# Performance work log

Hardware: AMD Instinct MI355X
Metric: run time of the kernel (lower is better)

The kernel has to match this reference:

```python
import jax, jax.numpy as jnp
import numpy as np

D = 1024
H = 16
HD = D // H
EPS = 1e-5
NEG = -1e20


def _layernorm(x, w, b):
    m = jnp.mean(x, axis=-1, keepdims=True)
    v = jnp.mean((x - m) ** 2, axis=-1, keepdims=True)
    return (x - m) * jax.lax.rsqrt(v + EPS) * w + b


def setup_inputs() -> dict:
    key = jax.random.key(0)
    ks = jax.random.split(key, 16)
    s = 0.02
    inp = {
        "X": jax.random.normal(ks[0], (2, 2048, D), jnp.float32),
        "Wq": jax.random.normal(ks[1], (D, D), jnp.float32) * s,
        "bq": jnp.zeros((D,), jnp.float32),
        "Wk": jax.random.normal(ks[2], (D, D), jnp.float32) * s,
        "bk": jnp.zeros((D,), jnp.float32),
        "Wv": jax.random.normal(ks[3], (D, D), jnp.float32) * s,
        "bv": jnp.zeros((D,), jnp.float32),
        "Wo": jax.random.normal(ks[4], (D, D), jnp.float32) * s,
        "bo": jnp.zeros((D,), jnp.float32),
        "ln1_w": jnp.ones((D,), jnp.float32),
        "ln1_b": jnp.zeros((D,), jnp.float32),
        "Wup": jax.random.normal(ks[5], (4 * D, D), jnp.float32) * s,
        "bup": jnp.zeros((4 * D,), jnp.float32),
        "Wdown": jax.random.normal(ks[6], (D, 4 * D), jnp.float32) * s,
        "bdown": jnp.zeros((D,), jnp.float32),
        "ln2_w": jnp.ones((D,), jnp.float32),
        "ln2_b": jnp.zeros((D,), jnp.float32),
    }
    return inp


def reference(X, Wq, bq, Wk, bk, Wv, bv, Wo, bo, ln1_w, ln1_b,
              Wup, bup, Wdown, bdown, ln2_w, ln2_b):
    B, S, _ = X.shape
    # QKV projections -> [B, H, S, HD]
    q = (X @ Wq.T + bq).reshape(B, S, H, HD).transpose(0, 2, 1, 3)
    k = (X @ Wk.T + bk).reshape(B, S, H, HD).transpose(0, 2, 1, 3)
    v = (X @ Wv.T + bv).reshape(B, S, H, HD).transpose(0, 2, 1, 3)
    scores = jnp.einsum("bhqd,bhkd->bhqk", q, k) / jnp.sqrt(jnp.float32(HD))
    causal = jnp.tril(jnp.ones((S, S), dtype=bool))  # mask==0 -> -1e20
    scores = jnp.where(causal, scores, jnp.float32(NEG))
    attn = jax.nn.softmax(scores, axis=-1)  # dropout is identity in eval
    out = jnp.einsum("bhqk,bhkd->bhqd", attn, v)
    out = out.transpose(0, 2, 1, 3).reshape(B, S, D)
    out = out @ Wo.T + bo
    x = _layernorm(X + out, ln1_w, ln1_b)  # post-LN attention block
    up = jax.nn.relu(x @ Wup.T + bup)
    down = up @ Wdown.T + bdown
    return _layernorm(x + down, ln2_w, ln2_b)
```

## Files before the change

### kernel.cpp

```cpp
#include <hip/hip_runtime.h>
#include <stdint.h>

#define DMODEL 1024
#define NHEAD 16
#define HDIM 64
#define SEQ 2048
#define NBATCH 2
#define MTOK 4096

typedef float f32x4 __attribute__((ext_vector_type(4)));
typedef short s16x8 __attribute__((ext_vector_type(8)));
typedef unsigned short u16;
typedef u16 u16x4 __attribute__((ext_vector_type(4)));

typedef __attribute__((address_space(1))) const void* as1_cvp;
typedef __attribute__((address_space(3))) void* as3_vp;

__device__ inline u16 f2bf(float f) {
  uint32_t u = __float_as_uint(f);
  u = u + 0x7FFFu + ((u >> 16) & 1u);
  return (u16)(u >> 16);
}

__device__ inline void gload_lds16(const void* g, void* l) {
  __builtin_amdgcn_global_load_lds((as1_cvp)g, (as3_vp)l, 16, 0, 0);
}

__global__ __launch_bounds__(256) void k_f2bf(const float* __restrict__ src,
                                              u16* __restrict__ dst, int n4) {
  int i = blockIdx.x * 256 + threadIdx.x;
  int stride = gridDim.x * 256;
  for (; i < n4; i += stride) {
    f32x4 v = ((const f32x4*)src)[i];
    u16x4 o;
    o[0] = f2bf(v[0]); o[1] = f2bf(v[1]); o[2] = f2bf(v[2]); o[3] = f2bf(v[3]);
    ((u16x4*)dst)[i] = o;
  }
}

__global__ __launch_bounds__(256) void k_f2bf_w4(
    const float* __restrict__ s0, const float* __restrict__ s1,
    const float* __restrict__ s2, const float* __restrict__ s3,
    u16* __restrict__ d0, u16* __restrict__ d1, u16* __restrict__ d2,
    u16* __restrict__ d3, int n4) {
  const float* src = blockIdx.y == 0 ? s0 : blockIdx.y == 1 ? s1
                     : blockIdx.y == 2 ? s2 : s3;
  u16* dst = blockIdx.y == 0 ? d0 : blockIdx.y == 1 ? d1
             : blockIdx.y == 2 ? d2 : d3;
  int i = blockIdx.x * 256 + threadIdx.x;
  int stride = gridDim.x * 256;
  for (; i < n4; i += stride) {
    f32x4 v = ((const f32x4*)src)[i];
    u16x4 o;
    o[0] = f2bf(v[0]); o[1] = f2bf(v[1]); o[2] = f2bf(v[2]); o[3] = f2bf(v[3]);
    ((u16x4*)dst)[i] = o;
  }
}

template <int MODE, int KSPL, int MH>
__global__ __launch_bounds__(512, 2) void k_gemm256(
    const u16* __restrict__ A, const u16* __restrict__ B,
    const float* __restrict__ bias, void* __restrict__ Cv,
    void* __restrict__ Cv1, int M, int N, int K) {
  constexpr int HALVES = MH + 2;
  __shared__ alignas(16) u16 lds[2 * HALVES * 8192];
  const int t = threadIdx.x;
  const int w = t >> 6;
  const int l = t & 63;
  const int wr = w >> 2;
  const int wc = w & 3;
  const int lr = l & 15, lg = l >> 4;
  const int r7 = lr & 7;
  const int lrow8 = l >> 3;

  const int gx = gridDim.x;
  int lin = blockIdx.y * gx + blockIdx.x;
  const int nwg = gx * gridDim.y;
  lin = (lin & 7) * (nwg >> 3) + (lin >> 3);
  const int bx = lin % gx, by = lin / gx;
  const int kz = KSPL > 1 ? blockIdx.z : 0;
  const int Kc = K / KSPL, kbeg = kz * Kc;
  const int brow = by * (MH * 128), bcol = bx * 256;

  constexpr int MF = MH * 4;
  const f32x4 Z4 = {0.f, 0.f, 0.f, 0.f};
  f32x4 acc[MF][4];
#pragma unroll
  for (int m = 0; m < MF; m++)
#pragma unroll
    for (int n = 0; n < 4; n++) acc[m][n] = Z4;

  const u16* Ag = A + (size_t)brow * K + kbeg;
  const u16* Bg = B + (size_t)bcol * K + kbeg;
  const int swz_src = ((l & 7) ^ ((l >> 3) & 7)) << 3;

  auto ldsH = [&](int buf, int half) { return lds + (buf * HALVES + half) * 8192; };
  auto stageA = [&](int kt, int buf) {
#pragma unroll
    for (int h = 0; h < MH; h++) {
      u16* lb = ldsH(buf, h);
      const int rb = h * 128;
      gload_lds16(Ag + (size_t)(rb + w * 8 + lrow8) * K + kt * 64 + swz_src,
                  lb + w * 512);
      gload_lds16(Ag + (size_t)(rb + 64 + w * 8 + lrow8) * K + kt * 64 + swz_src,
                  lb + (8 + w) * 512);
    }
  };
  auto stageB = [&](int kt, int buf) {
#pragma unroll
    for (int h = 0; h < 2; h++) {
      u16* lb = ldsH(buf, MH + h);
      const int rb = h * 128;
      gload_lds16(Bg + (size_t)(rb + w * 8 + lrow8) * K + kt * 64 + swz_src,
                  lb + w * 512);
      gload_lds16(Bg + (size_t)(rb + 64 + w * 8 + lrow8) * K + kt * 64 + swz_src,
                  lb + (8 + w) * 512);
    }
  };

  stageA(0, 0);
  stageB(0, 0);

  const int nkt = Kc >> 6;
  const int arb = (MH == 2) ? 0 : wr * 64;
  const int brb = (wc & 1) * 64;
  for (int kt = 0; kt < nkt; ++kt) {
    const int cur = kt & 1, nx = cur ^ 1;
    if (kt + 1 < nkt) {
      stageA(kt + 1, nx);
      if (MH == 2)
        asm volatile("s_waitcnt vmcnt(4)" ::: "memory");
      else
        asm volatile("s_waitcnt vmcnt(2)" ::: "memory");
    } else {
      asm volatile("s_waitcnt vmcnt(0)" ::: "memory");
    }
    __builtin_amdgcn_s_barrier();
    __builtin_amdgcn_sched_barrier(0);
    const u16* Ah = ldsH(cur, (MH == 2) ? wr : 0);
    const u16* Bh = ldsH(cur, MH + (wc >> 1));
#pragma unroll
    for (int kk = 0; kk < 2; kk++) {
      s16x8 bfr[4];
#pragma unroll
      for (int nf = 0; nf < 4; nf++)
        bfr[nf] = *(const s16x8*)(Bh + (brb + nf * 16 + lr) * 64 +
                                  (((kk * 4 + lg) ^ r7) << 3));
#pragma unroll
      for (int mh = 0; mh < MH; mh++) {
        s16x8 afr[4];
#pragma unroll
        for (int i = 0; i < 4; i++)
          afr[i] = *(const s16x8*)(Ah + (arb + (mh * 4 + i) * 16 + lr) * 64 +
                                   (((kk * 4 + lg) ^ r7) << 3));
        __builtin_amdgcn_s_setprio(1);
#pragma unroll
        for (int i = 0; i < 4; i++)
#pragma unroll
          for (int nf = 0; nf < 4; nf++)
            acc[mh * 4 + i][nf] = __builtin_amdgcn_mfma_f32_16x16x32_bf16(
                afr[i], bfr[nf], acc[mh * 4 + i][nf], 0, 0, 0);
        __builtin_amdgcn_s_setprio(0);
      }
      if (kk == 0 && kt + 1 < nkt) stageB(kt + 1, nx);
    }
    __builtin_amdgcn_sched_barrier(0);
    __builtin_amdgcn_s_barrier();
  }

  const int lg4 = lg * 4;
  const int wrb = wr * (MH == 2 ? 128 : 64);
  if (MODE == 0) {
    float* Co = (kz == 0) ? (float*)Cv : (float*)Cv1;
#pragma unroll
    for (int nf = 0; nf < 4; nf++) {
      const int col = bcol + wc * 64 + nf * 16 + lr;
      const float bvv = (kz == 0) ? bias[col] : 0.0f;
#pragma unroll
      for (int mf = 0; mf < MF; mf++) {
        const int row0 = brow + wrb + mf * 16 + lg4;
#pragma unroll
        for (int r = 0; r < 4; r++)
          Co[(size_t)(row0 + r) * N + col] = acc[mf][nf][r] + bvv;
      }
    }
  } else {
    u16* Sgw = lds + w * 2176;
    float bn[4];
#pragma unroll
    for (int nf = 0; nf < 4; nf++) bn[nf] = bias[bcol + wc * 64 + nf * 16 + lr];
    const int ch = l & 7;
#pragma unroll
    for (int hh = 0; hh < MH * 2; hh++) {
#pragma unroll
      for (int mm = 0; mm < 2; mm++) {
        const int mf = hh * 2 + mm;
#pragma unroll
        for (int nf = 0; nf < 4; nf++)
#pragma unroll
          for (int r = 0; r < 4; r++) {
            float vv = acc[mf][nf][r] + bn[nf];
            if (MODE == 2) vv = vv > 0.f ? vv : 0.f;
            Sgw[(mm * 16 + lg4 + r) * 68 + nf * 16 + lr] = f2bf(vv);
          }
      }
#pragma unroll
      for (int i = 0; i < 4; i++) {
        const int rr = i * 8 + (l >> 3);
        u16x4 a0 = *(const u16x4*)(Sgw + rr * 68 + ch * 8);
        u16x4 a1 = *(const u16x4*)(Sgw + rr * 68 + ch * 8 + 4);
        s16x8 v8;
#pragma unroll
        for (int j = 0; j < 4; j++) { v8[j] = (short)a0[j]; v8[4 + j] = (short)a1[j]; }
        *(s16x8*)((u16*)Cv + (size_t)(brow + wrb + hh * 32 + rr) * N +
                  (bcol + wc * 64 + ch * 8)) = v8;
      }
    }
  }
}

__global__ __launch_bounds__(256, 3) void k_gemm_qkv(
    const u16* __restrict__ A, const u16* __restrict__ B,
    const float* __restrict__ bq, const float* __restrict__ bk,
    const float* __restrict__ bv, u16* __restrict__ qbf, u16* __restrict__ kbf,
    u16* __restrict__ vtbf, int M, int N, int K) {
  __shared__ alignas(16) u16 As[2][128 * 32];
  __shared__ alignas(16) u16 Bs[2][128 * 32];
  __shared__ alignas(16) u16 Sg[4][32][68];
  const int t = threadIdx.x;
  const int w = t >> 6;
  const int l = t & 63;
  const int brow = blockIdx.y * 128;
  const int bcol = blockIdx.x * 128;
  const int wr = (w >> 1) * 64;
  const int wc = (w & 1) * 64;

  const f32x4 Z4 = {0.f, 0.f, 0.f, 0.f};
  f32x4 acc[4][4];
  for (int m = 0; m < 4; m++)
    for (int n = 0; n < 4; n++) acc[m][n] = Z4;

  const int sr = t >> 2;
  const int sc = (t & 3) * 8;
  const u16* Ab = A + (size_t)(brow + sr) * K + sc;
  const u16* Bb = B + (size_t)(bcol + sr) * K + sc;

  const int lr = l & 15;
  const int lk = (l >> 4) * 8;

  gload_lds16(Ab, &As[0][0] + w * 512);
  gload_lds16(Ab + (size_t)64 * K, &As[0][0] + 2048 + w * 512);
  gload_lds16(Bb, &Bs[0][0] + w * 512);
  gload_lds16(Bb + (size_t)64 * K, &Bs[0][0] + 2048 + w * 512);

  const int nk = K / 32;
  int cur = 0;
  for (int kt = 0; kt < nk; ++kt) {
    if (kt + 1 < nk) {
      const int k0 = (kt + 1) * 32;
      const int nx = cur ^ 1;
      gload_lds16(Ab + k0, &As[nx][0] + w * 512);
      gload_lds16(Ab + k0 + (size_t)64 * K, &As[nx][0] + 2048 + w * 512);
      gload_lds16(Bb + k0, &Bs[nx][0] + w * 512);
      gload_lds16(Bb + k0 + (size_t)64 * K, &Bs[nx][0] + 2048 + w * 512);
      asm volatile("s_waitcnt vmcnt(4)" ::: "memory");
    } else {
      asm volatile("s_waitcnt vmcnt(0)" ::: "memory");
    }
    __builtin_amdgcn_s_barrier();
    __builtin_amdgcn_sched_barrier(0);
    s16x8 af[4], bf[4];
    for (int m = 0; m < 4; m++)
      af[m] = *(const s16x8*)(&As[cur][0] + (wr + m * 16 + lr) * 32 + lk);
    for (int n = 0; n < 4; n++)
      bf[n] = *(const s16x8*)(&Bs[cur][0] + (wc + n * 16 + lr) * 32 + lk);
    for (int m = 0; m < 4; m++)
      for (int n = 0; n < 4; n++)
        acc[m][n] = __builtin_amdgcn_mfma_f32_16x16x32_bf16(af[m], bf[n],
                                                            acc[m][n], 0, 0, 0);
    __builtin_amdgcn_sched_barrier(0);
    __builtin_amdgcn_s_barrier();
    cur ^= 1;
  }

  const int lg = (l >> 4) * 4;
  const int region = bcol >> 10;
  float bn[4];
  {
    const float* bb = region == 0 ? bq : region == 1 ? bk : bv;
    for (int n = 0; n < 4; n++) bn[n] = bb[(bcol + wc + n * 16 + lr) & 1023];
  }
  if (region <= 1) {
    for (int hh = 0; hh < 2; hh++) {
      for (int mm = 0; mm < 2; mm++) {
        const int m = 2 * hh + mm;
        for (int n = 0; n < 4; n++)
          for (int r = 0; r < 4; r++) {
            float vv = acc[m][n][r] + bn[n];
            if (region == 0) vv *= 0.125f;
            Sg[w][mm * 16 + lg + r][n * 16 + lr] = f2bf(vv);
          }
      }
      const int ch = l & 7;
      for (int i = 0; i < 4; i++) {
        const int rr = i * 8 + (l >> 3);
        u16x4 a0 = *(const u16x4*)&Sg[w][rr][ch * 8];
        u16x4 a1 = *(const u16x4*)&Sg[w][rr][ch * 8 + 4];
        s16x8 v8;
        for (int j = 0; j < 4; j++) { v8[j] = (short)a0[j]; v8[4 + j] = (short)a1[j]; }
        const int tok = brow + wr + hh * 32 + rr;
        if (region == 0) {
          *(s16x8*)(qbf + (size_t)tok * 1024 + bcol + wc + ch * 8) = v8;
        } else {
          const int colb = bcol - 1024 + wc;
          *(s16x8*)(kbf + (size_t)tok * 1024 + colb + (((ch ^ tok) & 7) << 3)) =
              v8;
        }
      }
    }
  } else {
    for (int hh = 0; hh < 2; hh++) {
      for (int nn = 0; nn < 2; nn++) {
        const int n = 2 * hh + nn;
        for (int m = 0; m < 4; m++)
          for (int r = 0; r < 4; r++)
            Sg[w][nn * 16 + lr][m * 16 + lg + r] = f2bf(acc[m][n][r] + bn[n]);
      }
      const int ch = l & 7;
      const int hcol = (bcol - 2048 + wc) >> 6;
      for (int i = 0; i < 4; i++) {
        const int rr = i * 8 + (l >> 3);
        u16x4 a0 = *(const u16x4*)&Sg[w][rr][ch * 8];
        u16x4 a1 = *(const u16x4*)&Sg[w][rr][ch * 8 + 4];
        s16x8 v8;
        for (int j = 0; j < 4; j++) { v8[j] = (short)a0[j]; v8[4 + j] = (short)a1[j]; }
        const int d = hh * 32 + rr;
        const int tokb = brow + wr + ch * 8;
        const int b = tokb >> 11, s64b = tokb & 2047;
        const int ssb = (s64b & ~63) + ((((s64b >> 3) ^ d) & 7) << 3);
        *(s16x8*)(vtbf + ((size_t)((b << 4) + hcol) * 64 + d) * 2048 + ssb) = v8;
      }
    }
  }
}

__global__ __launch_bounds__(256, 2) void k_attn(const u16* __restrict__ q,
                                                 const u16* __restrict__ kk,
                                                 const u16* __restrict__ vt,
                                                 u16* __restrict__ o) {
  __shared__ alignas(16) u16 Ks[2][64 * 64];
  __shared__ alignas(16) u16 Vs[2][64 * 64];
  __shared__ alignas(16) u16 Ps[4 * 16 * 64];
  const int t = threadIdx.x;
  const int w = t >> 6;
  const int l = t & 63;
  const int idx = blockIdx.x;
  const int bh = idx & 31;
  const int p = idx >> 5;
  const int pm = p >> 3, pj = p & 7;
  const int qt = pm * 8 + ((pm & 1) ? (7 - pj) : pj);
  const int b = bh >> 4, h = bh & 15;
  const u16* qb = q + (size_t)b * SEQ * DMODEL + h * HDIM;
  const u16* kb = kk + (size_t)b * SEQ * DMODEL + h * HDIM;
  const u16* vb = vt + (size_t)((b * 16 + h) * 64) * SEQ;

  const int sr = t >> 3;
  const int sc = (t & 7) * 8;
  gload_lds16(qb + (size_t)(qt * 64 + sr) * DMODEL + sc, Ps + w * 512);
  gload_lds16(qb + (size_t)(qt * 64 + sr + 32) * DMODEL + sc,
              Ps + 2048 + w * 512);
  gload_lds16(kb + (size_t)sr * DMODEL + sc, &Ks[0][0] + w * 512);
  gload_lds16(kb + (size_t)(sr + 32) * DMODEL + sc, &Ks[0][0] + 2048 + w * 512);
  gload_lds16(vb + (size_t)sr * SEQ + sc, &Vs[0][0] + w * 512);
  gload_lds16(vb + (size_t)(sr + 32) * SEQ + sc, &Vs[0][0] + 2048 + w * 512);

  const int lr = l & 15, lg = l >> 4;
  const int key = lr & 7;
  const f32x4 Z4 = {0.f, 0.f, 0.f, 0.f};
  float m_l = -3.0e38f, l_l = 0.f;
  f32x4 oacc[4];
  for (int m = 0; m < 4; m++) oacc[m] = Z4;
  s16x8 bq0, bq1;
  u16* PsW = Ps + w * 1024;

  for (int jt = 0; jt <= qt; jt++) {
    const int cur = jt & 1;
    if (jt < qt) {
      const int nx = cur ^ 1;
      gload_lds16(kb + (size_t)((jt + 1) * 64 + sr) * DMODEL + sc,
                  &Ks[nx][0] + w * 512);
      gload_lds16(kb + (size_t)((jt + 1) * 64 + sr + 32) * DMODEL + sc,
                  &Ks[nx][0] + 2048 + w * 512);
      gload_lds16(vb + (size_t)sr * SEQ + (jt + 1) * 64 + sc,
                  &Vs[nx][0] + w * 512);
      gload_lds16(vb + (size_t)(sr + 32) * SEQ + (jt + 1) * 64 + sc,
                  &Vs[nx][0] + 2048 + w * 512);
      asm volatile("s_waitcnt vmcnt(4)" ::: "memory");
    } else {
      asm volatile("s_waitcnt vmcnt(0)" ::: "memory");
    }
    __builtin_amdgcn_s_barrier();
    __builtin_amdgcn_sched_barrier(0);
    const u16* Kc = &Ks[cur][0];
    const u16* Vc = &Vs[cur][0];
    if (jt == 0) {
      bq0 = *(const s16x8*)(Ps + (w * 16 + lr) * 64 + lg * 8);
      bq1 = *(const s16x8*)(Ps + (w * 16 + lr) * 64 + 32 + lg * 8);
    }
    f32x4 sacc[4];
    for (int m = 0; m < 4; m++) sacc[m] = Z4;
    for (int m = 0; m < 4; m++) {
      s16x8 ak0 = *(const s16x8*)(Kc + (m * 16 + lr) * 64 + ((lg ^ key) << 3));
      s16x8 ak1 =
          *(const s16x8*)(Kc + (m * 16 + lr) * 64 + (((4 | lg) ^ key) << 3));
      sacc[m] = __builtin_amdgcn_mfma_f32_16x16x32_bf16(ak0, bq0, sacc[m], 0, 0, 0);
      sacc[m] = __builtin_amdgcn_mfma_f32_16x16x32_bf16(ak1, bq1, sacc[m], 0, 0, 0);
    }
    if (jt == qt) {
      const int q_rel = w * 16 + lr;
      for (int m = 0; m < 4; m++)
        for (int r = 0; r < 4; r++)
          if (m * 16 + lg * 4 + r > q_rel) sacc[m][r] = -3.0e38f;
    }
    float tmax = -3.0e38f;
    for (int m = 0; m < 4; m++)
      for (int r = 0; r < 4; r++) tmax = fmaxf(tmax, sacc[m][r]);
    tmax = fmaxf(tmax, __shfl_xor(tmax, 16, 64));
    tmax = fmaxf(tmax, __shfl_xor(tmax, 32, 64));
    const float m_new = fmaxf(m_l, tmax);
    const float alpha = __expf(m_l - m_new);
    m_l = m_new;
    float p_[4][4];
    float rs = 0.f;
    for (int m = 0; m < 4; m++)
      for (int r = 0; r < 4; r++) {
        const float e = __expf(sacc[m][r] - m_new);
        p_[m][r] = e;
        rs += e;
      }
    rs += __shfl_xor(rs, 16, 64);
    rs += __shfl_xor(rs, 32, 64);
    l_l = l_l * alpha + rs;
    for (int m = 0; m < 4; m++)
      for (int r = 0; r < 4; r++) oacc[m][r] *= alpha;
    for (int m = 0; m < 4; m++)
      for (int pr = 0; pr < 2; pr++) {
        const uint32_t pk = (uint32_t)f2bf(p_[m][2 * pr]) |
                            ((uint32_t)f2bf(p_[m][2 * pr + 1]) << 16);
        const int kv0 = m * 16 + lg * 4 + 2 * pr;
        ((uint32_t*)PsW)[lr * 32 + (((kv0 >> 3) ^ key) << 2) +
                         ((kv0 >> 1) & 3)] = pk;
      }
    __builtin_amdgcn_sched_barrier(0);
    s16x8 bp0 = *(const s16x8*)(PsW + lr * 64 + ((lg ^ key) << 3));
    s16x8 bp1 = *(const s16x8*)(PsW + lr * 64 + (((4 | lg) ^ key) << 3));
    for (int m = 0; m < 4; m++) {
      s16x8 av0 = *(const s16x8*)(Vc + (m * 16 + lr) * 64 + ((lg ^ key) << 3));
      s16x8 av1 =
          *(const s16x8*)(Vc + (m * 16 + lr) * 64 + (((4 | lg) ^ key) << 3));
      oacc[m] = __builtin_amdgcn_mfma_f32_16x16x32_bf16(av0, bp0, oacc[m], 0, 0, 0);
      oacc[m] = __builtin_amdgcn_mfma_f32_16x16x32_bf16(av1, bp1, oacc[m], 0, 0, 0);
    }
    __builtin_amdgcn_sched_barrier(0);
    __builtin_amdgcn_s_barrier();
  }
  const float rl = 1.0f / l_l;
  const int tok = qt * 64 + w * 16 + lr;
  u16* orow = o + (size_t)(b * SEQ + tok) * DMODEL + h * HDIM;
  for (int m = 0; m < 4; m++)
    for (int pr = 0; pr < 2; pr++) {
      const uint32_t pk = (uint32_t)f2bf(oacc[m][2 * pr] * rl) |
                          ((uint32_t)f2bf(oacc[m][2 * pr + 1] * rl) << 16);
      *(uint32_t*)(orow + m * 16 + lg * 4 + 2 * pr) = pk;
    }
}

__global__ __launch_bounds__(256) void k_add_ln(const float* __restrict__ X,
                                                const float* __restrict__ Y,
                                                const float* __restrict__ Y1,
                                                const float* __restrict__ w,
                                                const float* __restrict__ bias,
                                                float* __restrict__ of32,
                                                u16* __restrict__ obf) {
  __shared__ float sred[4];
  const int t = threadIdx.x;
  const size_t row = blockIdx.x;
  f32x4 xv = ((const f32x4*)(X + row * DMODEL))[t];
  f32x4 yv = ((const f32x4*)(Y + row * DMODEL))[t];
  f32x4 vv;
  for (int i = 0; i < 4; i++) vv[i] = xv[i] + yv[i];
  if (Y1) {
    f32x4 y1 = ((const f32x4*)(Y1 + row * DMODEL))[t];
    for (int i = 0; i < 4; i++) vv[i] += y1[i];
  }
  float s = vv[0] + vv[1] + vv[2] + vv[3];
  for (int off = 32; off >= 1; off >>= 1) s += __shfl_xor(s, off, 64);
  if ((t & 63) == 0) sred[t >> 6] = s;
  __syncthreads();
  s = sred[0] + sred[1] + sred[2] + sred[3];
  const float mean = s * (1.0f / DMODEL);
  f32x4 dv;
  for (int i = 0; i < 4; i++) dv[i] = vv[i] - mean;
  float ss = dv[0] * dv[0] + dv[1] * dv[1] + dv[2] * dv[2] + dv[3] * dv[3];
  __syncthreads();
  for (int off = 32; off >= 1; off >>= 1) ss += __shfl_xor(ss, off, 64);
  if ((t & 63) == 0) sred[t >> 6] = ss;
  __syncthreads();
  ss = sred[0] + sred[1] + sred[2] + sred[3];
  const float rs = rsqrtf(ss * (1.0f / DMODEL) + 1e-5f);
  f32x4 wv = ((const f32x4*)w)[t];
  f32x4 bv = ((const f32x4*)bias)[t];
  f32x4 ov;
  for (int i = 0; i < 4; i++) ov[i] = dv[i] * rs * wv[i] + bv[i];
  if (of32) ((f32x4*)(of32 + row * DMODEL))[t] = ov;
  if (obf) {
    u16x4 ob;
    for (int i = 0; i < 4; i++) ob[i] = f2bf(ov[i]);
    ((u16x4*)(obf + row * DMODEL))[t] = ob;
  }
}

extern "C" void kernel_launch(void* const* d_in, const int* in_sizes, int n_in,
                              void* d_out, int out_size, void* d_ws,
                              size_t ws_size, hipStream_t stream) {
  const float* X = (const float*)d_in[0];
  const float* Wq = (const float*)d_in[1];
  const float* bq = (const float*)d_in[2];
  const float* Wk = (const float*)d_in[3];
  const float* bk = (const float*)d_in[4];
  const float* Wv = (const float*)d_in[5];
  const float* bvp = (const float*)d_in[6];
  const float* Wo = (const float*)d_in[7];
  const float* bo = (const float*)d_in[8];
  const float* ln1w = (const float*)d_in[9];
  const float* ln1b = (const float*)d_in[10];
  const float* Wup = (const float*)d_in[11];
  const float* bup = (const float*)d_in[12];
  const float* Wdown = (const float*)d_in[13];
  const float* bdown = (const float*)d_in[14];
  const float* ln2w = (const float*)d_in[15];
  const float* ln2b = (const float*)d_in[16];

  char* ws = (char*)d_ws;
  const size_t MB = 1024 * 1024;
  u16* Xbf = (u16*)(ws + 0);
  u16* qbf = (u16*)(ws + 8 * MB);
  u16* kbf = (u16*)(ws + 16 * MB);
  u16* vtbf = (u16*)(ws + 24 * MB);
  u16* wqkv = (u16*)(ws + 32 * MB);
  u16* wo = (u16*)(ws + 38 * MB);
  u16* attnb = (u16*)(ws + 40 * MB);
  float* Ybuf = (float*)(ws + 48 * MB);
  float* xres = (float*)(ws + 64 * MB);
  u16* xbf = (u16*)(ws + 80 * MB);
  u16* upbf = (u16*)(ws + 0);
  u16* wbig = (u16*)(ws + 32 * MB);
  float* Ypart = (float*)d_out;

  const dim3 blk(256);
  k_f2bf<<<2048, blk, 0, stream>>>(X, Xbf, (MTOK * DMODEL) / 4);
  k_f2bf_w4<<<dim3(512, 4), blk, 0, stream>>>(
      Wq, Wk, Wv, Wo, wqkv + 0 * 1024 * 1024, wqkv + 1 * 1024 * 1024,
      wqkv + 2 * 1024 * 1024, wo, (DMODEL * DMODEL) / 4);

  const dim3 gqkv(3 * DMODEL / 128, MTOK / 128);
  k_gemm_qkv<<<gqkv, blk, 0, stream>>>(Xbf, wqkv, bq, bk, bvp, qbf, kbf, vtbf,
                                       MTOK, 3 * DMODEL, DMODEL);
  k_attn<<<NBATCH * NHEAD * (SEQ / 64), blk, 0, stream>>>(qbf, kbf, vtbf, attnb);
  k_gemm256<0, 2, 1><<<dim3(4, 32, 2), dim3(512), 0, stream>>>(
      attnb, wo, bo, Ybuf, Ypart, MTOK, DMODEL, DMODEL);
  k_add_ln<<<MTOK, blk, 0, stream>>>(X, Ybuf, Ypart, ln1w, ln1b, xres, xbf);

  k_f2bf<<<2048, blk, 0, stream>>>(Wup, wbig, (4 * DMODEL * DMODEL) / 4);
  k_gemm256<2, 1, 2><<<dim3(16, 16), dim3(512), 0, stream>>>(
      xbf, wbig, bup, upbf, nullptr, MTOK, 4 * DMODEL, DMODEL);
  k_f2bf<<<2048, blk, 0, stream>>>(Wdown, wbig, (4 * DMODEL * DMODEL) / 4);
  k_gemm256<0, 2, 1><<<dim3(4, 32, 2), dim3(512), 0, stream>>>(
      upbf, wbig, bdown, Ybuf, Ypart, MTOK, DMODEL, 4 * DMODEL);
  k_add_ln<<<MTOK, blk, 0, stream>>>(xres, Ybuf, Ypart, ln2w, ln2b,
                                     (float*)d_out, (u16*)nullptr);
}
```

Baseline: 216.8 us.

## Retile QKV GEMM to 128x256 swizzled tiles and add lazy softmax rescale

Replaces the 128x128, 256-thread QKV projection GEMM with a 512-thread 128x256 tile kernel. It uses K=64 stages, XOR-swizzled LDS, split A/B prefetch interleaved with the MFMA work, s_setprio around the MFMAs, and a grouped block-index remap for L2 locality. The attention kernel's online softmax now rescales the running max and accumulators only when some lane's new max exceeds the old one by more than 8. This skips the exp and multiplies on most tiles, at the risk of larger intermediate exponentials (bounded by e^8) in bf16/fp32.

```diff
diff --git a/kernel.cpp b/kernel.cpp
--- a/kernel.cpp
+++ b/kernel.cpp
@@ -219,123 +219,169 @@
   }
 }
 
-__global__ __launch_bounds__(256, 3) void k_gemm_qkv(
+__global__ __launch_bounds__(512, 2) void k_gemm256_qkv(
     const u16* __restrict__ A, const u16* __restrict__ B,
     const float* __restrict__ bq, const float* __restrict__ bk,
     const float* __restrict__ bv, u16* __restrict__ qbf, u16* __restrict__ kbf,
     u16* __restrict__ vtbf, int M, int N, int K) {
-  __shared__ alignas(16) u16 As[2][128 * 32];
-  __shared__ alignas(16) u16 Bs[2][128 * 32];
-  __shared__ alignas(16) u16 Sg[4][32][68];
+  __shared__ alignas(16) u16 lds[2 * 3 * 8192];
   const int t = threadIdx.x;
-  const int w = t >> 6;
-  const int l = t & 63;
-  const int brow = blockIdx.y * 128;
-  const int bcol = blockIdx.x * 128;
-  const int wr = (w >> 1) * 64;
-  const int wc = (w & 1) * 64;
+  const int w = t >> 6, l = t & 63;
+  const int wr = w >> 2, wc = w & 3;
+  const int lr = l & 15, lg = l >> 4;
+  const int r7 = lr & 7;
+  const int lrow8 = l >> 3;
+
+  const int gx = gridDim.x;
+  int lin = blockIdx.y * gx + blockIdx.x;
+  const int nwg = gx * gridDim.y;
+  lin = (lin & 7) * (nwg >> 3) + (lin >> 3);
+  const int bx = lin % gx, by = lin / gx;
+  const int brow = by * 128, bcol = bx * 256;
 
   const f32x4 Z4 = {0.f, 0.f, 0.f, 0.f};
   f32x4 acc[4][4];
+#pragma unroll
   for (int m = 0; m < 4; m++)
+#pragma unroll
     for (int n = 0; n < 4; n++) acc[m][n] = Z4;
 
-  const int sr = t >> 2;
-  const int sc = (t & 3) * 8;
-  const u16* Ab = A + (size_t)(brow + sr) * K + sc;
-  const u16* Bb = B + (size_t)(bcol + sr) * K + sc;
-
-  const int lr = l & 15;
-  const int lk = (l >> 4) * 8;
-
-  gload_lds16(Ab, &As[0][0] + w * 512);
-  gload_lds16(Ab + (size_t)64 * K, &As[0][0] + 2048 + w * 512);
-  gload_lds16(Bb, &Bs[0][0] + w * 512);
-  gload_lds16(Bb + (size_t)64 * K, &Bs[0][0] + 2048 + w * 512);
-
-  const int nk = K / 32;
-  int cur = 0;
-  for (int kt = 0; kt < nk; ++kt) {
-    if (kt + 1 < nk) {
-      const int k0 = (kt + 1) * 32;
-      const int nx = cur ^ 1;
-      gload_lds16(Ab + k0, &As[nx][0] + w * 512);
-      gload_lds16(Ab + k0 + (size_t)64 * K, &As[nx][0] + 2048 + w * 512);
-      gload_lds16(Bb + k0, &Bs[nx][0] + w * 512);
-      gload_lds16(Bb + k0 + (size_t)64 * K, &Bs[nx][0] + 2048 + w * 512);
-      asm volatile("s_waitcnt vmcnt(4)" ::: "memory");
+  const u16* Ag = A + (size_t)brow * K;
+  const u16* Bg = B + (size_t)bcol * K;
+  const int swz_src = ((l & 7) ^ ((l >> 3) & 7)) << 3;
+
+  auto ldsH = [&](int buf, int half) { return lds + (buf * 3 + half) * 8192; };
+  auto stageA = [&](int kt, int buf) {
+    u16* lb = ldsH(buf, 0);
+    gload_lds16(Ag + (size_t)(w * 8 + lrow8) * K + kt * 64 + swz_src,
+                lb + w * 512);
+    gload_lds16(Ag + (size_t)(64 + w * 8 + lrow8) * K + kt * 64 + swz_src,
+                lb + (8 + w) * 512);
+  };
+  auto stageB = [&](int kt, int buf) {
+#pragma unroll
+    for (int h = 0; h < 2; h++) {
+      u16* lb = ldsH(buf, 1 + h);
+      const int rb = h * 128;
+      gload_lds16(Bg + (size_t)(rb + w * 8 + lrow8) * K + kt * 64 + swz_src,
+                  lb + w * 512);
+      gload_lds16(Bg + (size_t)(rb + 64 + w * 8 + lrow8) * K + kt * 64 + swz_src,
+                  lb + (8 + w) * 512);
+    }
+  };
+
+  stageA(0, 0);
+  stageB(0, 0);
+
+  const int nkt = K >> 6;
+  const int arb = wr * 64;
+  const int brb = (wc & 1) * 64;
+  for (int kt = 0; kt < nkt; ++kt) {
+    const int cur = kt & 1, nx = cur ^ 1;
+    if (kt + 1 < nkt) {
+      stageA(kt + 1, nx);
+      asm volatile("s_waitcnt vmcnt(2)" ::: "memory");
     } else {
       asm volatile("s_waitcnt vmcnt(0)" ::: "memory");
     }
     __builtin_amdgcn_s_barrier();
     __builtin_amdgcn_sched_barrier(0);
-    s16x8 af[4], bf[4];
-    for (int m = 0; m < 4; m++)
-      af[m] = *(const s16x8*)(&As[cur][0] + (wr + m * 16 + lr) * 32 + lk);
-    for (int n = 0; n < 4; n++)
-      bf[n] = *(const s16x8*)(&Bs[cur][0] + (wc + n * 16 + lr) * 32 + lk);
-    for (int m = 0; m < 4; m++)
-      for (int n = 0; n < 4; n++)
-        acc[m][n] = __builtin_amdgcn_mfma_f32_16x16x32_bf16(af[m], bf[n],
-                                                            acc[m][n], 0, 0, 0);
+    const u16* Ah = ldsH(cur, 0);
+    const u16* Bh = ldsH(cur, 1 + (wc >> 1));
+#pragma unroll
+    for (int kk = 0; kk < 2; kk++) {
+      s16x8 bfr[4];
+#pragma unroll
+      for (int nf = 0; nf < 4; nf++)
+        bfr[nf] = *(const s16x8*)(Bh + (brb + nf * 16 + lr) * 64 +
+                                  (((kk * 4 + lg) ^ r7) << 3));
+      s16x8 afr[4];
+#pragma unroll
+      for (int i = 0; i < 4; i++)
+        afr[i] = *(const s16x8*)(Ah + (arb + i * 16 + lr) * 64 +
+                                 (((kk * 4 + lg) ^ r7) << 3));
+      __builtin_amdgcn_s_setprio(1);
+#pragma unroll
+      for (int i = 0; i < 4; i++)
+#pragma unroll
+        for (int nf = 0; nf < 4; nf++)
+          acc[i][nf] = __builtin_amdgcn_mfma_f32_16x16x32_bf16(
+              afr[i], bfr[nf], acc[i][nf], 0, 0, 0);
+      __builtin_amdgcn_s_setprio(0);
+      if (kk == 0 && kt + 1 < nkt) stageB(kt + 1, nx);
+    }
     __builtin_amdgcn_sched_barrier(0);
     __builtin_amdgcn_s_barrier();
-    cur ^= 1;
-  }
-
-  const int lg = (l >> 4) * 4;
-  const int region = bcol >> 10;
+  }
+
+  const int lg4 = lg * 4;
+  const int wrb = wr * 64;
+  u16* Sgw = lds + w * 2176;
+  const int colw = bcol + wc * 64;
+  const int region = colw >> 10;
+  const int ck0 = colw & 1023;
   float bn[4];
   {
     const float* bb = region == 0 ? bq : region == 1 ? bk : bv;
-    for (int n = 0; n < 4; n++) bn[n] = bb[(bcol + wc + n * 16 + lr) & 1023];
-  }
+#pragma unroll
+    for (int nf = 0; nf < 4; nf++) bn[nf] = bb[ck0 + nf * 16 + lr];
+  }
+  const int ch = l & 7;
   if (region <= 1) {
+#pragma unroll
     for (int hh = 0; hh < 2; hh++) {
+#pragma unroll
       for (int mm = 0; mm < 2; mm++) {
-        const int m = 2 * hh + mm;
-        for (int n = 0; n < 4; n++)
+        const int mf = hh * 2 + mm;
+#pragma unroll
+        for (int nf = 0; nf < 4; nf++)
+#pragma unroll
           for (int r = 0; r < 4; r++) {
-            float vv = acc[m][n][r] + bn[n];
+            float vv = acc[mf][nf][r] + bn[nf];
             if (region == 0) vv *= 0.125f;
-            Sg[w][mm * 16 + lg + r][n * 16 + lr] = f2bf(vv);
+            Sgw[(mm * 16 + lg4 + r) * 68 + nf * 16 + lr] = f2bf(vv);
           }
       }
-      const int ch = l & 7;
+#pragma unroll
       for (int i = 0; i < 4; i++) {
         const int rr = i * 8 + (l >> 3);
-        u16x4 a0 = *(const u16x4*)&Sg[w][rr][ch * 8];
-        u16x4 a1 = *(const u16x4*)&Sg[w][rr][ch * 8 + 4];
+        u16x4 a0 = *(const u16x4*)(Sgw + rr * 68 + ch * 8);
+        u16x4 a1 = *(const u16x4*)(Sgw + rr * 68 + ch * 8 + 4);
         s16x8 v8;
+#pragma unroll
         for (int j = 0; j < 4; j++) { v8[j] = (short)a0[j]; v8[4 + j] = (short)a1[j]; }
-        const int tok = brow + wr + hh * 32 + rr;
-        if (region == 0) {
-          *(s16x8*)(qbf + (size_t)tok * 1024 + bcol + wc + ch * 8) = v8;
-        } else {
-          const int colb = bcol - 1024 + wc;
-          *(s16x8*)(kbf + (size_t)tok * 1024 + colb + (((ch ^ tok) & 7) << 3)) =
+        const int tok = brow + wrb + hh * 32 + rr;
+        if (region == 0)
+          *(s16x8*)(qbf + (size_t)tok * 1024 + ck0 + ch * 8) = v8;
+        else
+          *(s16x8*)(kbf + (size_t)tok * 1024 + ck0 + (((ch ^ tok) & 7) << 3)) =
               v8;
-        }
       }
     }
   } else {
+    const int hcol = ck0 >> 6;
+#pragma unroll
     for (int hh = 0; hh < 2; hh++) {
+#pragma unroll
       for (int nn = 0; nn < 2; nn++) {
-        const int n = 2 * hh + nn;
-        for (int m = 0; m < 4; m++)
+        const int nf = 2 * hh + nn;
+#pragma unroll
+        for (int mf = 0; mf < 4; mf++)
+#pragma unroll
           for (int r = 0; r < 4; r++)
-            Sg[w][nn * 16 + lr][m * 16 + lg + r] = f2bf(acc[m][n][r] + bn[n]);
-      }
-      const int ch = l & 7;
-      const int hcol = (bcol - 2048 + wc) >> 6;
+            Sgw[(nn * 16 + lr) * 68 + mf * 16 + lg4 + r] =
+                f2bf(acc[mf][nf][r] + bn[nf]);
+      }
+#pragma unroll
       for (int i = 0; i < 4; i++) {
         const int rr = i * 8 + (l >> 3);
-        u16x4 a0 = *(const u16x4*)&Sg[w][rr][ch * 8];
-        u16x4 a1 = *(const u16x4*)&Sg[w][rr][ch * 8 + 4];
+        u16x4 a0 = *(const u16x4*)(Sgw + rr * 68 + ch * 8);
+        u16x4 a1 = *(const u16x4*)(Sgw + rr * 68 + ch * 8 + 4);
         s16x8 v8;
+#pragma unroll
         for (int j = 0; j < 4; j++) { v8[j] = (short)a0[j]; v8[4 + j] = (short)a1[j]; }
         const int d = hh * 32 + rr;
-        const int tokb = brow + wr + ch * 8;
+        const int tokb = brow + wrb + ch * 8;
         const int b = tokb >> 11, s64b = tokb & 2047;
         const int ssb = (s64b & ~63) + ((((s64b >> 3) ^ d) & 7) << 3);
         *(s16x8*)(vtbf + ((size_t)((b << 4) + hcol) * 64 + d) * 2048 + ssb) = v8;
@@ -422,27 +468,30 @@
         for (int r = 0; r < 4; r++)
           if (m * 16 + lg * 4 + r > q_rel) sacc[m][r] = -3.0e38f;
     }
-    float tmax = -3.0e38f;
+    float mx[4];
     for (int m = 0; m < 4; m++)
-      for (int r = 0; r < 4; r++) tmax = fmaxf(tmax, sacc[m][r]);
-    tmax = fmaxf(tmax, __shfl_xor(tmax, 16, 64));
-    tmax = fmaxf(tmax, __shfl_xor(tmax, 32, 64));
-    const float m_new = fmaxf(m_l, tmax);
-    const float alpha = __expf(m_l - m_new);
-    m_l = m_new;
-    float p_[4][4];
-    float rs = 0.f;
-    for (int m = 0; m < 4; m++)
-      for (int r = 0; r < 4; r++) {
-        const float e = __expf(sacc[m][r] - m_new);
-        p_[m][r] = e;
-        rs += e;
-      }
+      mx[m] = fmaxf(fmaxf(sacc[m][0], sacc[m][1]),
+                    fmaxf(sacc[m][2], sacc[m][3]));
+    float pmax = fmaxf(fmaxf(mx[0], mx[1]), fmaxf(mx[2], mx[3]));
+    pmax = fmaxf(pmax, __shfl_xor(pmax, 16, 64));
+    pmax = fmaxf(pmax, __shfl_xor(pmax, 32, 64));
+    if (!__all(pmax - m_l <= 8.0f)) {
+      const float m_new = fmaxf(m_l, pmax);
+      const float alpha = __expf(m_l - m_new);
+      m_l = m_new;
+      l_l *= alpha;
+      for (int m = 0; m < 4; m++)
+        for (int r = 0; r < 4; r++) oacc[m][r] *= alpha;
+    }
+    float p_[4][4], sm[4];
+    for (int m = 0; m < 4; m++) {
+      for (int r = 0; r < 4; r++) p_[m][r] = __expf(sacc[m][r] - m_l);
+      sm[m] = (p_[m][0] + p_[m][1]) + (p_[m][2] + p_[m][3]);
+    }
+    float rs = (sm[0] + sm[1]) + (sm[2] + sm[3]);
     rs += __shfl_xor(rs, 16, 64);
     rs += __shfl_xor(rs, 32, 64);
-    l_l = l_l * alpha + rs;
-    for (int m = 0; m < 4; m++)
-      for (int r = 0; r < 4; r++) oacc[m][r] *= alpha;
+    l_l += rs;
     for (int m = 0; m < 4; m++)
       for (int pr = 0; pr < 2; pr++) {
         const uint32_t pk = (uint32_t)f2bf(p_[m][2 * pr]) |
@@ -563,9 +612,8 @@
       Wq, Wk, Wv, Wo, wqkv + 0 * 1024 * 1024, wqkv + 1 * 1024 * 1024,
       wqkv + 2 * 1024 * 1024, wo, (DMODEL * DMODEL) / 4);
 
-  const dim3 gqkv(3 * DMODEL / 128, MTOK / 128);
-  k_gemm_qkv<<<gqkv, blk, 0, stream>>>(Xbf, wqkv, bq, bk, bvp, qbf, kbf, vtbf,
-                                       MTOK, 3 * DMODEL, DMODEL);
+  k_gemm256_qkv<<<dim3(12, 32), dim3(512), 0, stream>>>(
+      Xbf, wqkv, bq, bk, bvp, qbf, kbf, vtbf, MTOK, 3 * DMODEL, DMODEL);
   k_attn<<<NBATCH * NHEAD * (SEQ / 64), blk, 0, stream>>>(qbf, kbf, vtbf, attnb);
   k_gemm256<0, 2, 1><<<dim3(4, 32, 2), dim3(512), 0, stream>>>(
       attnb, wo, bo, Ybuf, Ypart, MTOK, DMODEL, DMODEL);
```

Measured after the change: 220.9 us. Within noise of the previous version (+1.9%).

## Pair causal query tiles per block and add lazy softmax rescaling

Applied to the files above, without the earlier changes.

The attention kernel now launches half as many blocks. Each block processes two query tiles, p and 31-p, so every block does the same amount of causal work, which replaces the earlier serpentine tile ordering. The online softmax also skips rescaling the max and accumulator unless the new row max exceeds the running max by more than 8 anywhere in the wavefront. This saves exp and multiply work per tile. The risks are lower parallelism (512 blocks of 256 threads), serialisation of the two halves with no overlap of the second half's prologue, and a small change in numerics because stale maxima allow exponents up to e^8.

```diff
diff --git a/kernel.cpp b/kernel.cpp
--- a/kernel.cpp
+++ b/kernel.cpp
@@ -357,8 +357,6 @@
   const int idx = blockIdx.x;
   const int bh = idx & 31;
   const int p = idx >> 5;
-  const int pm = p >> 3, pj = p & 7;
-  const int qt = pm * 8 + ((pm & 1) ? (7 - pj) : pj);
   const int b = bh >> 4, h = bh & 15;
   const u16* qb = q + (size_t)b * SEQ * DMODEL + h * HDIM;
   const u16* kb = kk + (size_t)b * SEQ * DMODEL + h * HDIM;
@@ -366,113 +364,123 @@
 
   const int sr = t >> 3;
   const int sc = (t & 7) * 8;
-  gload_lds16(qb + (size_t)(qt * 64 + sr) * DMODEL + sc, Ps + w * 512);
-  gload_lds16(qb + (size_t)(qt * 64 + sr + 32) * DMODEL + sc,
-              Ps + 2048 + w * 512);
-  gload_lds16(kb + (size_t)sr * DMODEL + sc, &Ks[0][0] + w * 512);
-  gload_lds16(kb + (size_t)(sr + 32) * DMODEL + sc, &Ks[0][0] + 2048 + w * 512);
-  gload_lds16(vb + (size_t)sr * SEQ + sc, &Vs[0][0] + w * 512);
-  gload_lds16(vb + (size_t)(sr + 32) * SEQ + sc, &Vs[0][0] + 2048 + w * 512);
-
   const int lr = l & 15, lg = l >> 4;
   const int key = lr & 7;
   const f32x4 Z4 = {0.f, 0.f, 0.f, 0.f};
-  float m_l = -3.0e38f, l_l = 0.f;
-  f32x4 oacc[4];
-  for (int m = 0; m < 4; m++) oacc[m] = Z4;
-  s16x8 bq0, bq1;
   u16* PsW = Ps + w * 1024;
 
-  for (int jt = 0; jt <= qt; jt++) {
-    const int cur = jt & 1;
-    if (jt < qt) {
-      const int nx = cur ^ 1;
-      gload_lds16(kb + (size_t)((jt + 1) * 64 + sr) * DMODEL + sc,
-                  &Ks[nx][0] + w * 512);
-      gload_lds16(kb + (size_t)((jt + 1) * 64 + sr + 32) * DMODEL + sc,
-                  &Ks[nx][0] + 2048 + w * 512);
-      gload_lds16(vb + (size_t)sr * SEQ + (jt + 1) * 64 + sc,
-                  &Vs[nx][0] + w * 512);
-      gload_lds16(vb + (size_t)(sr + 32) * SEQ + (jt + 1) * 64 + sc,
-                  &Vs[nx][0] + 2048 + w * 512);
-      asm volatile("s_waitcnt vmcnt(4)" ::: "memory");
-    } else {
-      asm volatile("s_waitcnt vmcnt(0)" ::: "memory");
-    }
-    __builtin_amdgcn_s_barrier();
-    __builtin_amdgcn_sched_barrier(0);
-    const u16* Kc = &Ks[cur][0];
-    const u16* Vc = &Vs[cur][0];
-    if (jt == 0) {
-      bq0 = *(const s16x8*)(Ps + (w * 16 + lr) * 64 + lg * 8);
-      bq1 = *(const s16x8*)(Ps + (w * 16 + lr) * 64 + 32 + lg * 8);
-    }
-    f32x4 sacc[4];
-    for (int m = 0; m < 4; m++) sacc[m] = Z4;
-    for (int m = 0; m < 4; m++) {
-      s16x8 ak0 = *(const s16x8*)(Kc + (m * 16 + lr) * 64 + ((lg ^ key) << 3));
-      s16x8 ak1 =
-          *(const s16x8*)(Kc + (m * 16 + lr) * 64 + (((4 | lg) ^ key) << 3));
-      sacc[m] = __builtin_amdgcn_mfma_f32_16x16x32_bf16(ak0, bq0, sacc[m], 0, 0, 0);
-      sacc[m] = __builtin_amdgcn_mfma_f32_16x16x32_bf16(ak1, bq1, sacc[m], 0, 0, 0);
-    }
-    if (jt == qt) {
-      const int q_rel = w * 16 + lr;
+  for (int half = 0; half < 2; half++) {
+    const int qt = half ? (31 - p) : p;
+    gload_lds16(qb + (size_t)(qt * 64 + sr) * DMODEL + sc, Ps + w * 512);
+    gload_lds16(qb + (size_t)(qt * 64 + sr + 32) * DMODEL + sc,
+                Ps + 2048 + w * 512);
+    gload_lds16(kb + (size_t)sr * DMODEL + sc, &Ks[0][0] + w * 512);
+    gload_lds16(kb + (size_t)(sr + 32) * DMODEL + sc,
+                &Ks[0][0] + 2048 + w * 512);
+    gload_lds16(vb + (size_t)sr * SEQ + sc, &Vs[0][0] + w * 512);
+    gload_lds16(vb + (size_t)(sr + 32) * SEQ + sc, &Vs[0][0] + 2048 + w * 512);
+
+    float m_l = -3.0e38f, l_l = 0.f;
+    f32x4 oacc[4];
+    for (int m = 0; m < 4; m++) oacc[m] = Z4;
+    s16x8 bq0, bq1;
+
+    for (int jt = 0; jt <= qt; jt++) {
+      const int cur = jt & 1;
+      if (jt < qt) {
+        const int nx = cur ^ 1;
+        gload_lds16(kb + (size_t)((jt + 1) * 64 + sr) * DMODEL + sc,
+                    &Ks[nx][0] + w * 512);
+        gload_lds16(kb + (size_t)((jt + 1) * 64 + sr + 32) * DMODEL + sc,
+                    &Ks[nx][0] + 2048 + w * 512);
+        gload_lds16(vb + (size_t)sr * SEQ + (jt + 1) * 64 + sc,
+                    &Vs[nx][0] + w * 512);
+        gload_lds16(vb + (size_t)(sr + 32) * SEQ + (jt + 1) * 64 + sc,
+                    &Vs[nx][0] + 2048 + w * 512);
+        asm volatile("s_waitcnt vmcnt(4)" ::: "memory");
+      } else {
+        asm volatile("s_waitcnt vmcnt(0)" ::: "memory");
+      }
+      __builtin_amdgcn_s_barrier();
+      __builtin_amdgcn_sched_barrier(0);
+      const u16* Kc = &Ks[cur][0];
+      const u16* Vc = &Vs[cur][0];
+      if (jt == 0) {
+        bq0 = *(const s16x8*)(Ps + (w * 16 + lr) * 64 + lg * 8);
+        bq1 = *(const s16x8*)(Ps + (w * 16 + lr) * 64 + 32 + lg * 8);
+      }
+      f32x4 sacc[4];
+      for (int m = 0; m < 4; m++) sacc[m] = Z4;
+      for (int m = 0; m < 4; m++) {
+        s16x8 ak0 =
+            *(const s16x8*)(Kc + (m * 16 + lr) * 64 + ((lg ^ key) << 3));
+        s16x8 ak1 =
+            *(const s16x8*)(Kc + (m * 16 + lr) * 64 + (((4 | lg) ^ key) << 3));
+        sacc[m] = __builtin_amdgcn_mfma_f32_16x16x32_bf16(ak0, bq0, sacc[m], 0, 0, 0);
+        sacc[m] = __builtin_amdgcn_mfma_f32_16x16x32_bf16(ak1, bq1, sacc[m], 0, 0, 0);
+      }
+      if (jt == qt) {
+        const int q_rel = w * 16 + lr;
+        for (int m = 0; m < 4; m++)
+          for (int r = 0; r < 4; r++)
+            if (m * 16 + lg * 4 + r > q_rel) sacc[m][r] = -3.0e38f;
+      }
+      float mx[4];
       for (int m = 0; m < 4; m++)
-        for (int r = 0; r < 4; r++)
-          if (m * 16 + lg * 4 + r > q_rel) sacc[m][r] = -3.0e38f;
-    }
-    float tmax = -3.0e38f;
-    for (int m = 0; m < 4; m++)
-      for (int r = 0; r < 4; r++) tmax = fmaxf(tmax, sacc[m][r]);
-    tmax = fmaxf(tmax, __shfl_xor(tmax, 16, 64));
-    tmax = fmaxf(tmax, __shfl_xor(tmax, 32, 64));
-    const float m_new = fmaxf(m_l, tmax);
-    const float alpha = __expf(m_l - m_new);
-    m_l = m_new;
-    float p_[4][4];
-    float rs = 0.f;
-    for (int m = 0; m < 4; m++)
-      for (int r = 0; r < 4; r++) {
-        const float e = __expf(sacc[m][r] - m_new);
-        p_[m][r] = e;
-        rs += e;
-      }
-    rs += __shfl_xor(rs, 16, 64);
-    rs += __shfl_xor(rs, 32, 64);
-    l_l = l_l * alpha + rs;
-    for (int m = 0; m < 4; m++)
-      for (int r = 0; r < 4; r++) oacc[m][r] *= alpha;
+        mx[m] = fmaxf(fmaxf(sacc[m][0], sacc[m][1]),
+                      fmaxf(sacc[m][2], sacc[m][3]));
+      float pmax = fmaxf(fmaxf(mx[0], mx[1]), fmaxf(mx[2], mx[3]));
+      pmax = fmaxf(pmax, __shfl_xor(pmax, 16, 64));
+      pmax = fmaxf(pmax, __shfl_xor(pmax, 32, 64));
+      if (!__all(pmax - m_l <= 8.0f)) {
+        const float m_new = fmaxf(m_l, pmax);
+        const float alpha = __expf(m_l - m_new);
+        m_l = m_new;
+        l_l *= alpha;
+        for (int m = 0; m < 4; m++)
+          for (int r = 0; r < 4; r++) oacc[m][r] *= alpha;
+      }
+      float p_[4][4], sm[4];
+      for (int m = 0; m < 4; m++) {
+        for (int r = 0; r < 4; r++) p_[m][r] = __expf(sacc[m][r] - m_l);
+        sm[m] = (p_[m][0] + p_[m][1]) + (p_[m][2] + p_[m][3]);
+      }
+      float rs = (sm[0] + sm[1]) + (sm[2] + sm[3]);
+      rs += __shfl_xor(rs, 16, 64);
+      rs += __shfl_xor(rs, 32, 64);
+      l_l += rs;
+      for (int m = 0; m < 4; m++)
+        for (int pr = 0; pr < 2; pr++) {
+          const uint32_t pk = (uint32_t)f2bf(p_[m][2 * pr]) |
+                              ((uint32_t)f2bf(p_[m][2 * pr + 1]) << 16);
+          const int kv0 = m * 16 + lg * 4 + 2 * pr;
+          ((uint32_t*)PsW)[lr * 32 + (((kv0 >> 3) ^ key) << 2) +
+                           ((kv0 >> 1) & 3)] = pk;
+        }
+      __builtin_amdgcn_sched_barrier(0);
+      s16x8 bp0 = *(const s16x8*)(PsW + lr * 64 + ((lg ^ key) << 3));
+      s16x8 bp1 = *(const s16x8*)(PsW + lr * 64 + (((4 | lg) ^ key) << 3));
+      for (int m = 0; m < 4; m++) {
+        s16x8 av0 =
+            *(const s16x8*)(Vc + (m * 16 + lr) * 64 + ((lg ^ key) << 3));
+        s16x8 av1 =
+            *(const s16x8*)(Vc + (m * 16 + lr) * 64 + (((4 | lg) ^ key) << 3));
+        oacc[m] = __builtin_amdgcn_mfma_f32_16x16x32_bf16(av0, bp0, oacc[m], 0, 0, 0);
+        oacc[m] = __builtin_amdgcn_mfma_f32_16x16x32_bf16(av1, bp1, oacc[m], 0, 0, 0);
+      }
+      __builtin_amdgcn_sched_barrier(0);
+      __builtin_amdgcn_s_barrier();
+    }
+    const float rl = 1.0f / l_l;
+    const int tok = qt * 64 + w * 16 + lr;
+    u16* orow = o + (size_t)(b * SEQ + tok) * DMODEL + h * HDIM;
     for (int m = 0; m < 4; m++)
       for (int pr = 0; pr < 2; pr++) {
-        const uint32_t pk = (uint32_t)f2bf(p_[m][2 * pr]) |
-                            ((uint32_t)f2bf(p_[m][2 * pr + 1]) << 16);
-        const int kv0 = m * 16 + lg * 4 + 2 * pr;
-        ((uint32_t*)PsW)[lr * 32 + (((kv0 >> 3) ^ key) << 2) +
-                         ((kv0 >> 1) & 3)] = pk;
-      }
-    __builtin_amdgcn_sched_barrier(0);
-    s16x8 bp0 = *(const s16x8*)(PsW + lr * 64 + ((lg ^ key) << 3));
-    s16x8 bp1 = *(const s16x8*)(PsW + lr * 64 + (((4 | lg) ^ key) << 3));
-    for (int m = 0; m < 4; m++) {
-      s16x8 av0 = *(const s16x8*)(Vc + (m * 16 + lr) * 64 + ((lg ^ key) << 3));
-      s16x8 av1 =
-          *(const s16x8*)(Vc + (m * 16 + lr) * 64 + (((4 | lg) ^ key) << 3));
-      oacc[m] = __builtin_amdgcn_mfma_f32_16x16x32_bf16(av0, bp0, oacc[m], 0, 0, 0);
-      oacc[m] = __builtin_amdgcn_mfma_f32_16x16x32_bf16(av1, bp1, oacc[m], 0, 0, 0);
-    }
-    __builtin_amdgcn_sched_barrier(0);
-    __builtin_amdgcn_s_barrier();
-  }
-  const float rl = 1.0f / l_l;
-  const int tok = qt * 64 + w * 16 + lr;
-  u16* orow = o + (size_t)(b * SEQ + tok) * DMODEL + h * HDIM;
-  for (int m = 0; m < 4; m++)
-    for (int pr = 0; pr < 2; pr++) {
-      const uint32_t pk = (uint32_t)f2bf(oacc[m][2 * pr] * rl) |
-                          ((uint32_t)f2bf(oacc[m][2 * pr + 1] * rl) << 16);
-      *(uint32_t*)(orow + m * 16 + lg * 4 + 2 * pr) = pk;
-    }
+        const uint32_t pk = (uint32_t)f2bf(oacc[m][2 * pr] * rl) |
+                            ((uint32_t)f2bf(oacc[m][2 * pr + 1] * rl) << 16);
+        *(uint32_t*)(orow + m * 16 + lg * 4 + 2 * pr) = pk;
+      }
+  }
 }
 
 __global__ __launch_bounds__(256) void k_add_ln(const float* __restrict__ X,
@@ -566,7 +574,7 @@
   const dim3 gqkv(3 * DMODEL / 128, MTOK / 128);
   k_gemm_qkv<<<gqkv, blk, 0, stream>>>(Xbf, wqkv, bq, bk, bvp, qbf, kbf, vtbf,
                                        MTOK, 3 * DMODEL, DMODEL);
-  k_attn<<<NBATCH * NHEAD * (SEQ / 64), blk, 0, stream>>>(qbf, kbf, vtbf, attnb);
+  k_attn<<<16 * NBATCH * NHEAD, blk, 0, stream>>>(qbf, kbf, vtbf, attnb);
   k_gemm256<0, 2, 1><<<dim3(4, 32, 2), dim3(512), 0, stream>>>(
       attnb, wo, bo, Ybuf, Ypart, MTOK, DMODEL, DMODEL);
   k_add_ln<<<MTOK, blk, 0, stream>>>(X, Ybuf, Ypart, ln1w, ln1b, xres, xbf);
```

After: 216.4 us. About the same (-0.2%).
